# Kernel tuning notes

Hardware: AMD Instinct MI355X
Metric: run time of the kernel (lower is better)

The kernel has to match this reference:

```python
import jax, jax.numpy as jnp
import numpy as np

C_QKV = 128
C_HID = 32
N_HEADS = 4
INF = 1e9


def setup_inputs() -> dict:
    key = jax.random.key(0)
    ks = jax.random.split(key, 8)
    B, S = 256, 256
    hc = N_HEADS * C_HID  # 128
    inp = {
        "input_qkv": jax.random.normal(ks[0], (1, B, S, C_QKV), dtype=jnp.float32),
        "mask": jnp.ones((1, B, 1, 1, S), dtype=jnp.float32),
        "bias": jax.random.normal(ks[1], (1, 1, N_HEADS, S, S), dtype=jnp.float32),
        "add_transposed_output_to": jax.random.normal(ks[2], (1, B, S, C_QKV), dtype=jnp.float32),
        # linear_qkvg: Linear(c_qkv, 4*h*c), bias=False -> weight [4*hc, c_qkv]
        "W_qkvg": jax.random.normal(ks[3], (4 * hc, C_QKV), dtype=jnp.float32) * (1.0 / np.sqrt(C_QKV)),
        # gating bias initialized to ones in the module
        "linear_g_bias": jnp.ones((hc,), dtype=jnp.float32),
        # linear_o: Linear(hc, c_qkv), init='final' (zeros in AF2, use small random for a nontrivial test)
        "W_o": jax.random.normal(ks[4], (C_QKV, hc), dtype=jnp.float32) * (1.0 / np.sqrt(hc)),
        "b_o": jax.random.normal(ks[5], (C_QKV,), dtype=jnp.float32) * 0.02,
    }
    return inp


def reference(input_qkv, mask, bias, add_transposed_output_to, W_qkvg, linear_g_bias, W_o, b_o):
    hc = N_HEADS * C_HID
    # fused QKVG projection: [1, b, s, 4*hc]
    qkvg = jnp.einsum("xbsc,fc->xbsf", input_qkv, W_qkvg)
    q, k, v, g = jnp.split(qkvg, 4, axis=-1)
    # reshape to heads: [1, b, s, h, c]
    shp = q.shape[:-1] + (N_HEADS, C_HID)
    q = q.reshape(shp)
    k = k.reshape(shp)
    v = v.reshape(shp)
    scale = 1.0 / np.sqrt(C_HID)
    # scores: [1, b, h, q, k]
    a = jnp.einsum("xbqhc,xbkhc->xbhqk", q * scale, k)
    a = a + (mask - 1.0) * INF + bias
    a = jax.nn.softmax(a, axis=-1)
    # attention output: [1, b, q, h, c] -> [1, b, s, hc]
    o = jnp.einsum("xbhqk,xbkhc->xbqhc", a, v)
    o = o.reshape(o.shape[:-2] + (hc,))
    # sigmoid gating
    o = o * jax.nn.sigmoid(g + linear_g_bias)
    # fused linear + transpose(-2,-3) + add
    proj = jnp.einsum("xbsf,of->xbso", o, W_o) + b_o  # [1, b, s, c_qkv]
    out = add_transposed_output_to + jnp.swapaxes(proj, -2, -3)  # [1, s, b, c_qkv]
    return out
```

## Files before the change

### kernel.cpp

```cpp
#include <hip/hip_runtime.h>
#include <math.h>

#define BB 256
#define SS 256
#define NH 4

typedef __attribute__((ext_vector_type(8))) short bfrag;
typedef __attribute__((ext_vector_type(4))) float ffrag;

__device__ inline unsigned short f2bf(float x) {
    unsigned u = __float_as_uint(x);
    u += 0x7FFF + ((u >> 16) & 1);
    return (unsigned short)(u >> 16);
}
__device__ inline float bf2f(unsigned short h) {
    return __uint_as_float(((unsigned)h) << 16);
}
__device__ inline unsigned pack2(float a, float b) {
    return (unsigned)f2bf(a) | ((unsigned)f2bf(b) << 16);
}
__device__ inline bfrag pack_frag(float4 a, float4 b) {
    bfrag f;
    f[0] = (short)f2bf(a.x); f[1] = (short)f2bf(a.y);
    f[2] = (short)f2bf(a.z); f[3] = (short)f2bf(a.w);
    f[4] = (short)f2bf(b.x); f[5] = (short)f2bf(b.y);
    f[6] = (short)f2bf(b.z); f[7] = (short)f2bf(b.w);
    return f;
}
union FragU { unsigned u[4]; bfrag b; };

#define XB_OFF  0
#define WB_OFF  8388608
#define OG_OFF  8454144

__global__ __launch_bounds__(256) void k0_cast(
    const float* __restrict__ X, const float* __restrict__ W,
    unsigned short* __restrict__ dst)
{
    const int gid = blockIdx.x * 256 + threadIdx.x;
    const int XN8 = 8388608 / 8, WN8 = 65536 / 8;
    const float* src;
    size_t soff, doff;
    if (gid < XN8)            { src = X;  soff = (size_t)gid * 8;         doff = XB_OFF + soff; }
    else if (gid < XN8 + WN8) { src = W;  soff = (size_t)(gid - XN8) * 8; doff = WB_OFF + soff; }
    else return;
    const float4 a = *(const float4*)(src + soff);
    const float4 b = *(const float4*)(src + soff + 4);
    uint4 o;
    o.x = pack2(a.x, a.y); o.y = pack2(a.z, a.w);
    o.z = pack2(b.x, b.y); o.w = pack2(b.z, b.w);
    *(uint4*)(dst + doff) = o;
}

__global__ __launch_bounds__(512, 2) void k_fused(
    const unsigned short* __restrict__ Xb,
    const unsigned short* __restrict__ Wb,
    const float* __restrict__ gbias,
    const float* __restrict__ mask,
    const float* __restrict__ bias,
    unsigned short* __restrict__ og)
{
    const int b = blockIdx.x, h = blockIdx.y;
    const int t = threadIdx.x;
    const int w = t >> 6, lane = t & 63, l15 = lane & 15, quad = lane >> 4;

    __shared__ unsigned short Qb[SS * 40];
    __shared__ unsigned short Kb[SS * 40];
    __shared__ unsigned short Vt[32 * 264];
    __shared__ unsigned short Gb[SS * 34];
    __shared__ float maskLds[SS];

    if (t < SS) maskLds[t] = (mask[b * SS + t] - 1.0f) * 1e9f;

    const float qscale = 0.17677669529663687f;

    for (int half = 0; half < 2; ++half) {
        bfrag Wfr[4][4];
#pragma unroll
        for (int f4 = 0; f4 < 4; ++f4) {
            const int floc = (half * 4 + f4) * 16 + l15;
            const int grow = (floc >> 5) * 128 + h * 32 + (floc & 31);
#pragma unroll
            for (int cc = 0; cc < 4; ++cc)
                Wfr[f4][cc] = *(const bfrag*)(Wb + grow * 128 + cc * 32 + quad * 8);
        }
#pragma unroll
        for (int st = 0; st < 2; ++st) {
            const int s = w * 32 + st * 16 + l15;
            bfrag Xfr[4];
#pragma unroll
            for (int cc = 0; cc < 4; ++cc)
                Xfr[cc] = *(const bfrag*)(Xb + (b * SS + s) * 128 + cc * 32 + quad * 8);
#pragma unroll
            for (int f4 = 0; f4 < 4; ++f4) {
                ffrag D = {0.f, 0.f, 0.f, 0.f};
#pragma unroll
                for (int cc = 0; cc < 4; ++cc)
                    D = __builtin_amdgcn_mfma_f32_16x16x32_bf16(Xfr[cc], Wfr[f4][cc], D, 0, 0, 0);
                const int ft = half * 4 + f4;
                const int fcol = ft * 16 + l15;
                const int srow0 = w * 32 + st * 16 + quad * 4;
                if (ft < 2) {
#pragma unroll
                    for (int r = 0; r < 4; ++r)
                        Qb[(srow0 + r) * 40 + fcol] = f2bf(D[r] * qscale);
                } else if (ft < 4) {
#pragma unroll
                    for (int r = 0; r < 4; ++r)
                        Kb[(srow0 + r) * 40 + (fcol - 32)] = f2bf(D[r]);
                } else if (ft < 6) {
                    const int base = (fcol - 64) * 264 + srow0;
                    *(unsigned*)&Vt[base]     = pack2(D[0], D[1]);
                    *(unsigned*)&Vt[base + 2] = pack2(D[2], D[3]);
                } else {
                    const int c = fcol - 96;
                    const float gb = gbias[h * 32 + c];
#pragma unroll
                    for (int r = 0; r < 4; ++r) {
                        const float g = 1.0f / (1.0f + __expf(-(D[r] + gb)));
                        Gb[(srow0 + r) * 34 + c] = f2bf(g);
                    }
                }
            }
        }
    }
    __syncthreads();

    bfrag Vfr[2][8];
#pragma unroll
    for (int ch = 0; ch < 2; ++ch)
#pragma unroll
        for (int ck = 0; ck < 8; ++ck)
            Vfr[ch][ck] = *(const bfrag*)&Vt[(ch * 16 + l15) * 264 + ck * 32 + quad * 8];

    const int srcA = l15 + ((quad & 1) * 2) * 16;
    const int srcB = srcA + 16;
    const bool hi = (quad >> 1) != 0;

    for (int qq = 0; qq < 2; ++qq) {
        const int q = w * 32 + qq * 16 + l15;
        const bfrag Qfr = *(const bfrag*)&Qb[q * 40 + quad * 8];

        ffrag S[16];
#pragma unroll
        for (int kt = 0; kt < 16; ++kt) {
            const bfrag Kfr = *(const bfrag*)&Kb[(kt * 16 + l15) * 40 + quad * 8];
            const ffrag z = {0.f, 0.f, 0.f, 0.f};
            S[kt] = __builtin_amdgcn_mfma_f32_16x16x32_bf16(Kfr, Qfr, z, 0, 0, 0);
        }

        const float* brow = bias + (h * SS + q) * SS;
        float m = -1e30f;
#pragma unroll
        for (int kt = 0; kt < 16; ++kt) {
            const float4 bv = *(const float4*)(brow + kt * 16 + quad * 4);
            const float4 mv = *(const float4*)(maskLds + kt * 16 + quad * 4);
            S[kt][0] += bv.x + mv.x; S[kt][1] += bv.y + mv.y;
            S[kt][2] += bv.z + mv.z; S[kt][3] += bv.w + mv.w;
            m = fmaxf(m, fmaxf(fmaxf(S[kt][0], S[kt][1]), fmaxf(S[kt][2], S[kt][3])));
        }
        m = fmaxf(m, __shfl_xor(m, 16, 64));
        m = fmaxf(m, __shfl_xor(m, 32, 64));

        float l = 0.f;
        unsigned pk[16][2];
#pragma unroll
        for (int kt = 0; kt < 16; ++kt) {
            const float p0 = __expf(S[kt][0] - m);
            const float p1 = __expf(S[kt][1] - m);
            const float p2 = __expf(S[kt][2] - m);
            const float p3 = __expf(S[kt][3] - m);
            l += (p0 + p1) + (p2 + p3);
            pk[kt][0] = pack2(p0, p1);
            pk[kt][1] = pack2(p2, p3);
        }
        l += __shfl_xor(l, 16, 64);
        l += __shfl_xor(l, 32, 64);

        ffrag O[2];
        O[0] = (ffrag){0.f, 0.f, 0.f, 0.f};
        O[1] = (ffrag){0.f, 0.f, 0.f, 0.f};
#pragma unroll
        for (int ck = 0; ck < 8; ++ck) {
            const unsigned a0 = (unsigned)__shfl((int)pk[2 * ck][0],     srcA, 64);
            const unsigned b0 = (unsigned)__shfl((int)pk[2 * ck + 1][0], srcA, 64);
            const unsigned a1 = (unsigned)__shfl((int)pk[2 * ck][1],     srcA, 64);
            const unsigned b1 = (unsigned)__shfl((int)pk[2 * ck + 1][1], srcA, 64);
            const unsigned a2 = (unsigned)__shfl((int)pk[2 * ck][0],     srcB, 64);
            const unsigned b2 = (unsigned)__shfl((int)pk[2 * ck + 1][0], srcB, 64);
            const unsigned a3 = (unsigned)__shfl((int)pk[2 * ck][1],     srcB, 64);
            const unsigned b3 = (unsigned)__shfl((int)pk[2 * ck + 1][1], srcB, 64);
            FragU fu;
            fu.u[0] = hi ? b0 : a0;
            fu.u[1] = hi ? b1 : a1;
            fu.u[2] = hi ? b2 : a2;
            fu.u[3] = hi ? b3 : a3;
            O[0] = __builtin_amdgcn_mfma_f32_16x16x32_bf16(Vfr[0][ck], fu.b, O[0], 0, 0, 0);
            O[1] = __builtin_amdgcn_mfma_f32_16x16x32_bf16(Vfr[1][ck], fu.b, O[1], 0, 0, 0);
        }

        const float invl = 1.0f / l;
        const unsigned short* gr = &Gb[q * 34];
        unsigned* orow = (unsigned*)(og + ((size_t)b * SS + q) * 128 + h * 32);
#pragma unroll
        for (int ch = 0; ch < 2; ++ch) {
            const int c0 = ch * 16 + quad * 4;
            const float v0 = O[ch][0] * invl * bf2f(gr[c0 + 0]);
            const float v1 = O[ch][1] * invl * bf2f(gr[c0 + 1]);
            const float v2 = O[ch][2] * invl * bf2f(gr[c0 + 2]);
            const float v3 = O[ch][3] * invl * bf2f(gr[c0 + 3]);
            orow[(c0 >> 1) + 0] = pack2(v0, v1);
            orow[(c0 >> 1) + 1] = pack2(v2, v3);
        }
    }
}

__global__ __launch_bounds__(256, 4) void k3_proj(
    const unsigned short* __restrict__ ogb,
    const float* __restrict__ Wo,
    const float* __restrict__ bo,
    const float* __restrict__ addt,
    float* __restrict__ out)
{
    const int i = blockIdx.x, jt4 = blockIdx.y;
    const int t = threadIdx.x;
    const int w = t >> 6, lane = t & 63, l15 = lane & 15, quad = lane >> 4;

    __shared__ unsigned short OgS[64 * 136];

    {
        const int jj = t >> 2, part = t & 3;
        const unsigned short* src = ogb + ((size_t)(jt4 * 64 + jj) * SS + i) * 128 + part * 32;
        unsigned short* dst = &OgS[jj * 136 + part * 32];
        *(uint4*)(dst)      = *(const uint4*)(src);
        *(uint4*)(dst + 8)  = *(const uint4*)(src + 8);
        *(uint4*)(dst + 16) = *(const uint4*)(src + 16);
        *(uint4*)(dst + 24) = *(const uint4*)(src + 24);
    }

    bfrag Wfr[2][4];
#pragma unroll
    for (int ctl = 0; ctl < 2; ++ctl) {
        const int crow = (w * 2 + ctl) * 16 + l15;
#pragma unroll
        for (int cc = 0; cc < 4; ++cc) {
            const float* p = Wo + crow * 128 + cc * 32 + quad * 8;
            Wfr[ctl][cc] = pack_frag(*(const float4*)p, *(const float4*)(p + 4));
        }
    }
    const float bo0 = bo[(w * 2 + 0) * 16 + l15];
    const float bo1 = bo[(w * 2 + 1) * 16 + l15];

    __syncthreads();

#pragma unroll
    for (int jt = 0; jt < 4; ++jt) {
        bfrag Ab[4];
#pragma unroll
        for (int cc = 0; cc < 4; ++cc)
            Ab[cc] = *(const bfrag*)&OgS[(jt * 16 + l15) * 136 + cc * 32 + quad * 8];

        ffrag D0 = {0.f, 0.f, 0.f, 0.f};
        ffrag D1 = {0.f, 0.f, 0.f, 0.f};
#pragma unroll
        for (int cc = 0; cc < 4; ++cc) {
            D0 = __builtin_amdgcn_mfma_f32_16x16x32_bf16(Ab[cc], Wfr[0][cc], D0, 0, 0, 0);
            D1 = __builtin_amdgcn_mfma_f32_16x16x32_bf16(Ab[cc], Wfr[1][cc], D1, 0, 0, 0);
        }

        const int c0 = (w * 2 + 0) * 16 + l15;
        const int c1 = (w * 2 + 1) * 16 + l15;
#pragma unroll
        for (int r = 0; r < 4; ++r) {
            const int j = jt4 * 64 + jt * 16 + quad * 4 + r;
            const size_t row = (size_t)(i * BB + j) * 128;
            out[row + c0] = D0[r] + bo0 + addt[row + c0];
            out[row + c1] = D1[r] + bo1 + addt[row + c1];
        }
    }
}

extern "C" void kernel_launch(void* const* d_in, const int* in_sizes, int n_in,
                              void* d_out, int out_size, void* d_ws, size_t ws_size,
                              hipStream_t stream) {
    const float* X     = (const float*)d_in[0];
    const float* mask  = (const float*)d_in[1];
    const float* bias  = (const float*)d_in[2];
    const float* addt  = (const float*)d_in[3];
    const float* Wqkvg = (const float*)d_in[4];
    const float* gbias = (const float*)d_in[5];
    const float* Wo    = (const float*)d_in[6];
    const float* bo    = (const float*)d_in[7];
    float* out = (float*)d_out;

    unsigned short* ws = (unsigned short*)d_ws;
    unsigned short* Xb = ws + XB_OFF;
    unsigned short* Wb = ws + WB_OFF;
    unsigned short* og = ws + OG_OFF;

    k0_cast<<<4128, 256, 0, stream>>>(X, Wqkvg, ws);
    k_fused<<<dim3(BB, NH), 512, 0, stream>>>(Xb, Wb, gbias, mask, bias, og);
    k3_proj<<<dim3(SS, 4), 256, 0, stream>>>(og, Wo, bo, addt, out);
}
```

Baseline: 280.1 us.

## Fuse all heads and output projection into one per-batch attention kernel

Each block now handles one batch row across all four heads in a loop and keeps the gated attention output in LDS. It then applies the output projection, bias, transpose and residual add in the same kernel. The separate bf16 cast of X is dropped in favour of converting X in registers, and the global og intermediate is gone. This removes a full pass over X and a round-trip of the attention output through global memory. In exchange the grid shrinks to 256 large blocks with about 143KB of LDS each, which lowers occupancy and latency hiding, and V fragments are now reloaded from LDS inside the PV loop.

```diff
diff --git a/kernel.cpp b/kernel.cpp
--- a/kernel.cpp
+++ b/kernel.cpp
@@ -29,20 +29,19 @@
 }
 union FragU { unsigned u[4]; bfrag b; };
 
-#define XB_OFF  0
-#define WB_OFF  8388608
-#define OG_OFF  8454144
+#define WB_OFF  0
+#define WOB_OFF 65536
 
 __global__ __launch_bounds__(256) void k0_cast(
-    const float* __restrict__ X, const float* __restrict__ W,
+    const float* __restrict__ W, const float* __restrict__ Wo,
     unsigned short* __restrict__ dst)
 {
     const int gid = blockIdx.x * 256 + threadIdx.x;
-    const int XN8 = 8388608 / 8, WN8 = 65536 / 8;
+    const int WN8 = 65536 / 8, WoN8 = 16384 / 8;
     const float* src;
     size_t soff, doff;
-    if (gid < XN8)            { src = X;  soff = (size_t)gid * 8;         doff = XB_OFF + soff; }
-    else if (gid < XN8 + WN8) { src = W;  soff = (size_t)(gid - XN8) * 8; doff = WB_OFF + soff; }
+    if (gid < WN8)            { src = W;  soff = (size_t)gid * 8;         doff = WB_OFF + soff; }
+    else if (gid < WN8 + WoN8) { src = Wo; soff = (size_t)(gid - WN8) * 8; doff = WOB_OFF + soff; }
     else return;
     const float4 a = *(const float4*)(src + soff);
     const float4 b = *(const float4*)(src + soff + 4);
@@ -52,15 +51,18 @@
     *(uint4*)(dst + doff) = o;
 }
 
-__global__ __launch_bounds__(512, 2) void k_fused(
-    const unsigned short* __restrict__ Xb,
+__global__ __launch_bounds__(512, 2) void k_mega(
+    const float* __restrict__ X,
     const unsigned short* __restrict__ Wb,
     const float* __restrict__ gbias,
     const float* __restrict__ mask,
     const float* __restrict__ bias,
-    unsigned short* __restrict__ og)
+    const unsigned short* __restrict__ Wob,
+    const float* __restrict__ bo,
+    const float* __restrict__ addt,
+    float* __restrict__ out)
 {
-    const int b = blockIdx.x, h = blockIdx.y;
+    const int b = blockIdx.x;
     const int t = threadIdx.x;
     const int w = t >> 6, lane = t & 63, l15 = lane & 15, quad = lane >> 4;
 
@@ -68,214 +70,180 @@
     __shared__ unsigned short Kb[SS * 40];
     __shared__ unsigned short Vt[32 * 264];
     __shared__ unsigned short Gb[SS * 34];
+    __shared__ unsigned short OgL[SS * 132];
     __shared__ float maskLds[SS];
 
     if (t < SS) maskLds[t] = (mask[b * SS + t] - 1.0f) * 1e9f;
 
     const float qscale = 0.17677669529663687f;
 
-    for (int half = 0; half < 2; ++half) {
-        bfrag Wfr[4][4];
-#pragma unroll
-        for (int f4 = 0; f4 < 4; ++f4) {
-            const int floc = (half * 4 + f4) * 16 + l15;
-            const int grow = (floc >> 5) * 128 + h * 32 + (floc & 31);
-#pragma unroll
-            for (int cc = 0; cc < 4; ++cc)
-                Wfr[f4][cc] = *(const bfrag*)(Wb + grow * 128 + cc * 32 + quad * 8);
-        }
-#pragma unroll
-        for (int st = 0; st < 2; ++st) {
-            const int s = w * 32 + st * 16 + l15;
-            bfrag Xfr[4];
-#pragma unroll
-            for (int cc = 0; cc < 4; ++cc)
-                Xfr[cc] = *(const bfrag*)(Xb + (b * SS + s) * 128 + cc * 32 + quad * 8);
-#pragma unroll
-            for (int f4 = 0; f4 < 4; ++f4) {
-                ffrag D = {0.f, 0.f, 0.f, 0.f};
-#pragma unroll
-                for (int cc = 0; cc < 4; ++cc)
-                    D = __builtin_amdgcn_mfma_f32_16x16x32_bf16(Xfr[cc], Wfr[f4][cc], D, 0, 0, 0);
-                const int ft = half * 4 + f4;
-                const int fcol = ft * 16 + l15;
-                const int srow0 = w * 32 + st * 16 + quad * 4;
-                if (ft < 2) {
-#pragma unroll
-                    for (int r = 0; r < 4; ++r)
-                        Qb[(srow0 + r) * 40 + fcol] = f2bf(D[r] * qscale);
-                } else if (ft < 4) {
-#pragma unroll
-                    for (int r = 0; r < 4; ++r)
-                        Kb[(srow0 + r) * 40 + (fcol - 32)] = f2bf(D[r]);
-                } else if (ft < 6) {
-                    const int base = (fcol - 64) * 264 + srow0;
-                    *(unsigned*)&Vt[base]     = pack2(D[0], D[1]);
-                    *(unsigned*)&Vt[base + 2] = pack2(D[2], D[3]);
-                } else {
-                    const int c = fcol - 96;
-                    const float gb = gbias[h * 32 + c];
-#pragma unroll
-                    for (int r = 0; r < 4; ++r) {
-                        const float g = 1.0f / (1.0f + __expf(-(D[r] + gb)));
-                        Gb[(srow0 + r) * 34 + c] = f2bf(g);
-                    }
-                }
-            }
+    bfrag Xfr[2][4];
+#pragma unroll
+    for (int st = 0; st < 2; ++st) {
+        const int s = w * 32 + st * 16 + l15;
+#pragma unroll
+        for (int cc = 0; cc < 4; ++cc) {
+            const float* p = X + (b * SS + s) * 128 + cc * 32 + quad * 8;
+            Xfr[st][cc] = pack_frag(*(const float4*)p, *(const float4*)(p + 4));
         }
     }
-    __syncthreads();
-
-    bfrag Vfr[2][8];
-#pragma unroll
-    for (int ch = 0; ch < 2; ++ch)
-#pragma unroll
-        for (int ck = 0; ck < 8; ++ck)
-            Vfr[ch][ck] = *(const bfrag*)&Vt[(ch * 16 + l15) * 264 + ck * 32 + quad * 8];
 
     const int srcA = l15 + ((quad & 1) * 2) * 16;
     const int srcB = srcA + 16;
     const bool hi = (quad >> 1) != 0;
 
-    for (int qq = 0; qq < 2; ++qq) {
-        const int q = w * 32 + qq * 16 + l15;
-        const bfrag Qfr = *(const bfrag*)&Qb[q * 40 + quad * 8];
-
-        ffrag S[16];
-#pragma unroll
-        for (int kt = 0; kt < 16; ++kt) {
-            const bfrag Kfr = *(const bfrag*)&Kb[(kt * 16 + l15) * 40 + quad * 8];
-            const ffrag z = {0.f, 0.f, 0.f, 0.f};
-            S[kt] = __builtin_amdgcn_mfma_f32_16x16x32_bf16(Kfr, Qfr, z, 0, 0, 0);
-        }
-
-        const float* brow = bias + (h * SS + q) * SS;
-        float m = -1e30f;
-#pragma unroll
-        for (int kt = 0; kt < 16; ++kt) {
-            const float4 bv = *(const float4*)(brow + kt * 16 + quad * 4);
-            const float4 mv = *(const float4*)(maskLds + kt * 16 + quad * 4);
-            S[kt][0] += bv.x + mv.x; S[kt][1] += bv.y + mv.y;
-            S[kt][2] += bv.z + mv.z; S[kt][3] += bv.w + mv.w;
-            m = fmaxf(m, fmaxf(fmaxf(S[kt][0], S[kt][1]), fmaxf(S[kt][2], S[kt][3])));
-        }
-        m = fmaxf(m, __shfl_xor(m, 16, 64));
-        m = fmaxf(m, __shfl_xor(m, 32, 64));
-
-        float l = 0.f;
-        unsigned pk[16][2];
-#pragma unroll
-        for (int kt = 0; kt < 16; ++kt) {
-            const float p0 = __expf(S[kt][0] - m);
-            const float p1 = __expf(S[kt][1] - m);
-            const float p2 = __expf(S[kt][2] - m);
-            const float p3 = __expf(S[kt][3] - m);
-            l += (p0 + p1) + (p2 + p3);
-            pk[kt][0] = pack2(p0, p1);
-            pk[kt][1] = pack2(p2, p3);
-        }
-        l += __shfl_xor(l, 16, 64);
-        l += __shfl_xor(l, 32, 64);
-
-        ffrag O[2];
-        O[0] = (ffrag){0.f, 0.f, 0.f, 0.f};
-        O[1] = (ffrag){0.f, 0.f, 0.f, 0.f};
-#pragma unroll
-        for (int ck = 0; ck < 8; ++ck) {
-            const unsigned a0 = (unsigned)__shfl((int)pk[2 * ck][0],     srcA, 64);
-            const unsigned b0 = (unsigned)__shfl((int)pk[2 * ck + 1][0], srcA, 64);
-            const unsigned a1 = (unsigned)__shfl((int)pk[2 * ck][1],     srcA, 64);
-            const unsigned b1 = (unsigned)__shfl((int)pk[2 * ck + 1][1], srcA, 64);
-            const unsigned a2 = (unsigned)__shfl((int)pk[2 * ck][0],     srcB, 64);
-            const unsigned b2 = (unsigned)__shfl((int)pk[2 * ck + 1][0], srcB, 64);
-            const unsigned a3 = (unsigned)__shfl((int)pk[2 * ck][1],     srcB, 64);
-            const unsigned b3 = (unsigned)__shfl((int)pk[2 * ck + 1][1], srcB, 64);
-            FragU fu;
-            fu.u[0] = hi ? b0 : a0;
-            fu.u[1] = hi ? b1 : a1;
-            fu.u[2] = hi ? b2 : a2;
-            fu.u[3] = hi ? b3 : a3;
-            O[0] = __builtin_amdgcn_mfma_f32_16x16x32_bf16(Vfr[0][ck], fu.b, O[0], 0, 0, 0);
-            O[1] = __builtin_amdgcn_mfma_f32_16x16x32_bf16(Vfr[1][ck], fu.b, O[1], 0, 0, 0);
-        }
-
-        const float invl = 1.0f / l;
-        const unsigned short* gr = &Gb[q * 34];
-        unsigned* orow = (unsigned*)(og + ((size_t)b * SS + q) * 128 + h * 32);
-#pragma unroll
-        for (int ch = 0; ch < 2; ++ch) {
-            const int c0 = ch * 16 + quad * 4;
-            const float v0 = O[ch][0] * invl * bf2f(gr[c0 + 0]);
-            const float v1 = O[ch][1] * invl * bf2f(gr[c0 + 1]);
-            const float v2 = O[ch][2] * invl * bf2f(gr[c0 + 2]);
-            const float v3 = O[ch][3] * invl * bf2f(gr[c0 + 3]);
-            orow[(c0 >> 1) + 0] = pack2(v0, v1);
-            orow[(c0 >> 1) + 1] = pack2(v2, v3);
+    for (int h = 0; h < NH; ++h) {
+        __syncthreads();
+
+        for (int half = 0; half < 2; ++half) {
+            bfrag Wfr[4][4];
+#pragma unroll
+            for (int f4 = 0; f4 < 4; ++f4) {
+                const int floc = (half * 4 + f4) * 16 + l15;
+                const int grow = (floc >> 5) * 128 + h * 32 + (floc & 31);
+#pragma unroll
+                for (int cc = 0; cc < 4; ++cc)
+                    Wfr[f4][cc] = *(const bfrag*)(Wb + grow * 128 + cc * 32 + quad * 8);
+            }
+#pragma unroll
+            for (int st = 0; st < 2; ++st) {
+#pragma unroll
+                for (int f4 = 0; f4 < 4; ++f4) {
+                    ffrag D = {0.f, 0.f, 0.f, 0.f};
+#pragma unroll
+                    for (int cc = 0; cc < 4; ++cc)
+                        D = __builtin_amdgcn_mfma_f32_16x16x32_bf16(Xfr[st][cc], Wfr[f4][cc], D, 0, 0, 0);
+                    const int ft = half * 4 + f4;
+                    const int fcol = ft * 16 + l15;
+                    const int srow0 = w * 32 + st * 16 + quad * 4;
+                    if (ft < 2) {
+#pragma unroll
+                        for (int r = 0; r < 4; ++r)
+                            Qb[(srow0 + r) * 40 + fcol] = f2bf(D[r] * qscale);
+                    } else if (ft < 4) {
+#pragma unroll
+                        for (int r = 0; r < 4; ++r)
+                            Kb[(srow0 + r) * 40 + (fcol - 32)] = f2bf(D[r]);
+                    } else if (ft < 6) {
+                        const int base = (fcol - 64) * 264 + srow0;
+                        *(unsigned*)&Vt[base]     = pack2(D[0], D[1]);
+                        *(unsigned*)&Vt[base + 2] = pack2(D[2], D[3]);
+                    } else {
+                        const int c = fcol - 96;
+                        const float gb = gbias[h * 32 + c];
+#pragma unroll
+                        for (int r = 0; r < 4; ++r) {
+                            const float g = 1.0f / (1.0f + __expf(-(D[r] + gb)));
+                            Gb[(srow0 + r) * 34 + c] = f2bf(g);
+                        }
+                    }
+                }
+            }
+        }
+        __syncthreads();
+
+        for (int qq = 0; qq < 2; ++qq) {
+            const int q = w * 32 + qq * 16 + l15;
+            const bfrag Qfr = *(const bfrag*)&Qb[q * 40 + quad * 8];
+
+            ffrag S[16];
+#pragma unroll
+            for (int kt = 0; kt < 16; ++kt) {
+                const bfrag Kfr = *(const bfrag*)&Kb[(kt * 16 + l15) * 40 + quad * 8];
+                const ffrag z = {0.f, 0.f, 0.f, 0.f};
+                S[kt] = __builtin_amdgcn_mfma_f32_16x16x32_bf16(Kfr, Qfr, z, 0, 0, 0);
+            }
+
+            const float* brow = bias + (h * SS + q) * SS;
+            float m = -1e30f;
+#pragma unroll
+            for (int kt = 0; kt < 16; ++kt) {
+                const float4 bv = *(const float4*)(brow + kt * 16 + quad * 4);
+                const float4 mv = *(const float4*)(maskLds + kt * 16 + quad * 4);
+                S[kt][0] += bv.x + mv.x; S[kt][1] += bv.y + mv.y;
+                S[kt][2] += bv.z + mv.z; S[kt][3] += bv.w + mv.w;
+                m = fmaxf(m, fmaxf(fmaxf(S[kt][0], S[kt][1]), fmaxf(S[kt][2], S[kt][3])));
+            }
+            m = fmaxf(m, __shfl_xor(m, 16, 64));
+            m = fmaxf(m, __shfl_xor(m, 32, 64));
+
+            float l = 0.f;
+            unsigned pk[16][2];
+#pragma unroll
+            for (int kt = 0; kt < 16; ++kt) {
+                const float p0 = __expf(S[kt][0] - m);
+                const float p1 = __expf(S[kt][1] - m);
+                const float p2 = __expf(S[kt][2] - m);
+                const float p3 = __expf(S[kt][3] - m);
+                l += (p0 + p1) + (p2 + p3);
+                pk[kt][0] = pack2(p0, p1);
+                pk[kt][1] = pack2(p2, p3);
+            }
+            l += __shfl_xor(l, 16, 64);
+            l += __shfl_xor(l, 32, 64);
+
+            ffrag O[2];
+            O[0] = (ffrag){0.f, 0.f, 0.f, 0.f};
+            O[1] = (ffrag){0.f, 0.f, 0.f, 0.f};
+#pragma unroll
+            for (int ck = 0; ck < 8; ++ck) {
+                const unsigned a0 = (unsigned)__shfl((int)pk[2 * ck][0],     srcA, 64);
+                const unsigned b0 = (unsigned)__shfl((int)pk[2 * ck + 1][0], srcA, 64);
+                const unsigned a1 = (unsigned)__shfl((int)pk[2 * ck][1],     srcA, 64);
+                const unsigned b1 = (unsigned)__shfl((int)pk[2 * ck + 1][1], srcA, 64);
+                const unsigned a2 = (unsigned)__shfl((int)pk[2 * ck][0],     srcB, 64);
+                const unsigned b2 = (unsigned)__shfl((int)pk[2 * ck + 1][0], srcB, 64);
+                const unsigned a3 = (unsigned)__shfl((int)pk[2 * ck][1],     srcB, 64);
+                const unsigned b3 = (unsigned)__shfl((int)pk[2 * ck + 1][1], srcB, 64);
+                FragU fu;
+                fu.u[0] = hi ? b0 : a0;
+                fu.u[1] = hi ? b1 : a1;
+                fu.u[2] = hi ? b2 : a2;
+                fu.u[3] = hi ? b3 : a3;
+                const bfrag V0 = *(const bfrag*)&Vt[l15 * 264 + ck * 32 + quad * 8];
+                const bfrag V1 = *(const bfrag*)&Vt[(16 + l15) * 264 + ck * 32 + quad * 8];
+                O[0] = __builtin_amdgcn_mfma_f32_16x16x32_bf16(V0, fu.b, O[0], 0, 0, 0);
+                O[1] = __builtin_amdgcn_mfma_f32_16x16x32_bf16(V1, fu.b, O[1], 0, 0, 0);
+            }
+
+            const float invl = 1.0f / l;
+            const unsigned short* gr = &Gb[q * 34];
+            unsigned* orow = (unsigned*)&OgL[q * 132 + h * 32];
+#pragma unroll
+            for (int ch = 0; ch < 2; ++ch) {
+                const int c0 = ch * 16 + quad * 4;
+                const float v0 = O[ch][0] * invl * bf2f(gr[c0 + 0]);
+                const float v1 = O[ch][1] * invl * bf2f(gr[c0 + 1]);
+                const float v2 = O[ch][2] * invl * bf2f(gr[c0 + 2]);
+                const float v3 = O[ch][3] * invl * bf2f(gr[c0 + 3]);
+                orow[(c0 >> 1) + 0] = pack2(v0, v1);
+                orow[(c0 >> 1) + 1] = pack2(v2, v3);
+            }
         }
     }
-}
-
-__global__ __launch_bounds__(256, 4) void k3_proj(
-    const unsigned short* __restrict__ ogb,
-    const float* __restrict__ Wo,
-    const float* __restrict__ bo,
-    const float* __restrict__ addt,
-    float* __restrict__ out)
-{
-    const int i = blockIdx.x, jt4 = blockIdx.y;
-    const int t = threadIdx.x;
-    const int w = t >> 6, lane = t & 63, l15 = lane & 15, quad = lane >> 4;
-
-    __shared__ unsigned short OgS[64 * 136];
-
-    {
-        const int jj = t >> 2, part = t & 3;
-        const unsigned short* src = ogb + ((size_t)(jt4 * 64 + jj) * SS + i) * 128 + part * 32;
-        unsigned short* dst = &OgS[jj * 136 + part * 32];
-        *(uint4*)(dst)      = *(const uint4*)(src);
-        *(uint4*)(dst + 8)  = *(const uint4*)(src + 8);
-        *(uint4*)(dst + 16) = *(const uint4*)(src + 16);
-        *(uint4*)(dst + 24) = *(const uint4*)(src + 24);
-    }
-
-    bfrag Wfr[2][4];
-#pragma unroll
-    for (int ctl = 0; ctl < 2; ++ctl) {
-        const int crow = (w * 2 + ctl) * 16 + l15;
-#pragma unroll
-        for (int cc = 0; cc < 4; ++cc) {
-            const float* p = Wo + crow * 128 + cc * 32 + quad * 8;
-            Wfr[ctl][cc] = pack_frag(*(const float4*)p, *(const float4*)(p + 4));
-        }
-    }
-    const float bo0 = bo[(w * 2 + 0) * 16 + l15];
-    const float bo1 = bo[(w * 2 + 1) * 16 + l15];
-
-    __syncthreads();
-
-#pragma unroll
-    for (int jt = 0; jt < 4; ++jt) {
+
+#pragma unroll
+    for (int st = 0; st < 2; ++st) {
         bfrag Ab[4];
 #pragma unroll
         for (int cc = 0; cc < 4; ++cc)
-            Ab[cc] = *(const bfrag*)&OgS[(jt * 16 + l15) * 136 + cc * 32 + quad * 8];
-
-        ffrag D0 = {0.f, 0.f, 0.f, 0.f};
-        ffrag D1 = {0.f, 0.f, 0.f, 0.f};
-#pragma unroll
-        for (int cc = 0; cc < 4; ++cc) {
-            D0 = __builtin_amdgcn_mfma_f32_16x16x32_bf16(Ab[cc], Wfr[0][cc], D0, 0, 0, 0);
-            D1 = __builtin_amdgcn_mfma_f32_16x16x32_bf16(Ab[cc], Wfr[1][cc], D1, 0, 0, 0);
-        }
-
-        const int c0 = (w * 2 + 0) * 16 + l15;
-        const int c1 = (w * 2 + 1) * 16 + l15;
-#pragma unroll
-        for (int r = 0; r < 4; ++r) {
-            const int j = jt4 * 64 + jt * 16 + quad * 4 + r;
-            const size_t row = (size_t)(i * BB + j) * 128;
-            out[row + c0] = D0[r] + bo0 + addt[row + c0];
-            out[row + c1] = D1[r] + bo1 + addt[row + c1];
+            Ab[cc] = *(const bfrag*)&OgL[(w * 32 + st * 16 + l15) * 132 + cc * 32 + quad * 8];
+
+#pragma unroll
+        for (int ct = 0; ct < 8; ++ct) {
+            ffrag D = {0.f, 0.f, 0.f, 0.f};
+#pragma unroll
+            for (int cc = 0; cc < 4; ++cc) {
+                const bfrag Bf = *(const bfrag*)(Wob + (ct * 16 + l15) * 128 + cc * 32 + quad * 8);
+                D = __builtin_amdgcn_mfma_f32_16x16x32_bf16(Ab[cc], Bf, D, 0, 0, 0);
+            }
+            const float bov = bo[ct * 16 + l15];
+#pragma unroll
+            for (int r = 0; r < 4; ++r) {
+                const int s = w * 32 + st * 16 + quad * 4 + r;
+                const size_t idx = ((size_t)s * BB + b) * 128 + ct * 16 + l15;
+                out[idx] = D[r] + bov + addt[idx];
+            }
         }
     }
 }
@@ -293,12 +261,10 @@
     const float* bo    = (const float*)d_in[7];
     float* out = (float*)d_out;
 
-    unsigned short* ws = (unsigned short*)d_ws;
-    unsigned short* Xb = ws + XB_OFF;
-    unsigned short* Wb = ws + WB_OFF;
-    unsigned short* og = ws + OG_OFF;
-
-    k0_cast<<<4128, 256, 0, stream>>>(X, Wqkvg, ws);
-    k_fused<<<dim3(BB, NH), 512, 0, stream>>>(Xb, Wb, gbias, mask, bias, og);
-    k3_proj<<<dim3(SS, 4), 256, 0, stream>>>(og, Wo, bo, addt, out);
-}
+    unsigned short* ws  = (unsigned short*)d_ws;
+    unsigned short* Wb  = ws + WB_OFF;
+    unsigned short* Wob = ws + WOB_OFF;
+
+    k0_cast<<<40, 256, 0, stream>>>(Wqkvg, Wo, ws);
+    k_mega<<<BB, 512, 0, stream>>>(X, Wb, gbias, mask, bias, Wob, bo, addt, out);
+}
```

New measurement: 286.1 us. 2.1% more time.
